# Optimization experiments

Measured on AMD Instinct MI355X. Metric: run time of the kernel, lower is better.

## Reference

```python
import jax, jax.numpy as jnp
import numpy as np

V, NB, NJ, NP, NK = 6890, 10, 24, 207, 19
PARENTS = np.array([-1, 0, 0, 0, 1, 2, 3, 4, 5, 6, 7, 8, 9, 9, 9, 12, 13, 14, 16, 17, 18, 19, 20, 21])


def setup_inputs():
    key = jax.random.key(0)
    ks = jax.random.split(key, 9)
    B = 1024
    beta = jax.random.normal(ks[0], (B, NB), jnp.float32)
    theta = jax.random.normal(ks[1], (B, NJ * 3), jnp.float32) * 0.3  # axis-angle per joint
    trans = jax.random.normal(ks[2], (B, 3), jnp.float32)
    v_template = jax.random.normal(ks[3], (V, 3), jnp.float32)
    shapedirs = jax.random.normal(ks[4], (NB, V * 3), jnp.float32) * 0.03
    Jr = jax.random.uniform(ks[5], (V, NJ), jnp.float32)
    J_regressor = Jr / jnp.sum(Jr, axis=0, keepdims=True)
    posedirs = jax.random.normal(ks[6], (NP, V * 3), jnp.float32) * 0.01
    jr = jax.random.uniform(ks[7], (V, NK), jnp.float32)
    joint_regressor = jr / jnp.sum(jr, axis=0, keepdims=True)
    w = jax.random.uniform(ks[8], (V, NJ), jnp.float32)
    weights = w / jnp.sum(w, axis=1, keepdims=True)  # LBS weights, rows sum to 1
    return dict(beta=beta, theta=theta, trans=trans, v_template=v_template,
                shapedirs=shapedirs, J_regressor=J_regressor, posedirs=posedirs,
                joint_regressor=joint_regressor, weights=weights)


def batch_rodrigues(theta):
    # theta: (N,3) axis-angle -> (N,3,3) rotation matrices via quaternions (HMR-style)
    angle = jnp.linalg.norm(theta + 1e-8, axis=1, keepdims=True)
    half = angle * 0.5
    v = (theta / angle) * jnp.sin(half)
    quat = jnp.concatenate([jnp.cos(half), v], axis=1)
    quat = quat / jnp.linalg.norm(quat, axis=1, keepdims=True)
    w, x, y, z = quat[:, 0], quat[:, 1], quat[:, 2], quat[:, 3]
    rot = jnp.stack([
        1 - 2 * (y * y + z * z), 2 * (x * y - w * z), 2 * (x * z + w * y),
        2 * (x * y + w * z), 1 - 2 * (x * x + z * z), 2 * (y * z - w * x),
        2 * (x * z - w * y), 2 * (y * z + w * x), 1 - 2 * (x * x + y * y)], axis=1)
    return rot.reshape(-1, 3, 3)


def batch_global_rigid_transformation(Rs, J):
    # Rs: (B,24,3,3), J: (B,24,3); rotate_base=True
    B = Rs.shape[0]
    rot_x = jnp.array([[1., 0., 0.], [0., -1., 0.], [0., 0., -1.]], jnp.float32)
    root_R = Rs[:, 0] @ rot_x

    def make_A(R, t):  # (B,3,3),(B,3) -> (B,4,4)
        top = jnp.concatenate([R, t[:, :, None]], axis=2)
        bot = jnp.broadcast_to(jnp.array([0., 0., 0., 1.], jnp.float32), (B, 1, 4))
        return jnp.concatenate([top, bot], axis=1)

    results = [make_A(root_R, J[:, 0])]
    for i in range(1, NJ):  # fixed 24-joint kinematic chain
        t = J[:, i] - J[:, PARENTS[i]]
        results.append(results[PARENTS[i]] @ make_A(Rs[:, i], t))
    res = jnp.stack(results, axis=1)  # (B,24,4,4)
    new_J = res[:, :, :3, 3]
    j_w0 = jnp.concatenate([J, jnp.zeros_like(J[:, :, :1])], axis=2)  # (B,24,4), homo w=0
    init_bone = jnp.einsum('bjrc,bjc->bjr', res, j_w0)
    A = res.at[:, :, :, 3].add(-init_bone)  # subtract only last column (matches F.pad trick)
    return new_J, A


def reference(beta, theta, trans, v_template, shapedirs, J_regressor, posedirs, joint_regressor, weights):
    B = beta.shape[0]
    v_shaped = (beta @ shapedirs).reshape(B, V, 3) + v_template
    J = jnp.einsum('bvc,vj->bjc', v_shaped, J_regressor)  # (B,24,3)
    Rs = batch_rodrigues(theta.reshape(-1, 3)).reshape(B, NJ, 3, 3)
    pose_feature = (Rs[:, 1:] - jnp.eye(3, dtype=Rs.dtype)).reshape(B, NP)
    v_posed = (pose_feature @ posedirs).reshape(B, V, 3) + v_shaped
    _, A = batch_global_rigid_transformation(Rs, J)
    T = jnp.einsum('vj,bjrc->bvrc', weights, A)  # (B,V,4,4) per-vertex skinning transforms
    homo = jnp.concatenate([v_posed, jnp.ones((B, V, 1), v_posed.dtype)], axis=2)
    verts = jnp.einsum('bvrc,bvc->bvr', T, homo)[:, :, :3] + trans[:, None, :]
    joints = jnp.einsum('bvc,vk->bkc', verts, joint_regressor)  # (B,19,3)
    return joints
```

## Files before the change

### kernel.cpp

```cpp
#include <hip/hip_runtime.h>
#include <hip/hip_bf16.h>

constexpr int Vn   = 6890;
constexpr int VC3  = 20670;
constexpr int NKB  = 216;
constexpr int QT   = 224;
constexpr int NMG  = 14;
constexpr int NCOL = 480;
constexpr int WR   = 1440;
constexpr int MC   = 1368;
constexpr int KSEG = 8;
constexpr int RB   = 158;

using bf16x8  = __attribute__((ext_vector_type(8))) short;
using floatx4 = __attribute__((ext_vector_type(4))) float;

__device__ __forceinline__ unsigned short f2bf(float f) {
    unsigned int u = __float_as_uint(f);
    unsigned int r = (u + 0x7FFFu + ((u >> 16) & 1u)) >> 16;
    return (unsigned short)r;
}

__global__ __launch_bounds__(256) void k0_build(
    const float* __restrict__ vt, const float* __restrict__ sdirs,
    const float* __restrict__ pdirs, const float* __restrict__ Jreg,
    const float* __restrict__ jreg, const float* __restrict__ wts,
    unsigned short* __restrict__ Af, unsigned short* __restrict__ Bf,
    float* __restrict__ Jacc)
{
    int bx = blockIdx.x, t = threadIdx.x;
    if (bx < 756) {
        int g = bx * 256 + t;
        int q = g / 864, u = g % 864;
        int v0 = u * 8, base = 3 * v0;
        float buf[24];
        if (q == 0) {
            #pragma unroll
            for (int i = 0; i < 24; ++i) buf[i] = (v0 + i / 3 < Vn) ? 1.f : 0.f;
        } else {
            const float* src = nullptr;
            if (q == 1) src = vt;
            else if (q >= 2 && q < 12)   src = sdirs + (size_t)(q - 2) * VC3;
            else if (q >= 12 && q < 219) src = pdirs + (size_t)(q - 12) * VC3;
            if (src && base + 23 < VC3) {
                #pragma unroll
                for (int i = 0; i < 12; ++i) {
                    float2 f = *(const float2*)(src + base + 2 * i);
                    buf[2 * i] = f.x; buf[2 * i + 1] = f.y;
                }
            } else {
                #pragma unroll
                for (int i = 0; i < 24; ++i)
                    buf[i] = (src && base + i < VC3) ? src[base + i] : 0.f;
            }
        }
        int kb = u >> 2, quad = u & 3, mg = q >> 4;
        size_t foff = (size_t)((q & 15) + quad * 16) * 8;
        #pragma unroll
        for (int c = 0; c < 3; ++c) {
            bf16x8 o;
            #pragma unroll
            for (int j = 0; j < 8; ++j) o[j] = (short)f2bf(buf[3 * j + c]);
            *(bf16x8*)(Af + ((size_t)(c * NMG + mg) * NKB + kb) * 512 + foff) = o;
        }
        return;
    }
    bx -= 756;
    if (bx < 108) {
        int v0 = bx * 64;
        __shared__ float js[64 * 19], wsh[64 * 24], Jsh[64 * 24];
        for (int i = t; i < 64 * 19; i += 256)
            js[i] = (v0 * 19 + i < Vn * 19) ? jreg[v0 * 19 + i] : 0.f;
        for (int i = t; i < 64 * 24; i += 256) {
            wsh[i] = (v0 * 24 + i < Vn * 24) ? wts[v0 * 24 + i] : 0.f;
            Jsh[i] = (v0 * 24 + i < Vn * 24) ? Jreg[v0 * 24 + i] : 0.f;
        }
        __syncthreads();
        for (int s = t; s < 4096; s += 256) {
            int col = s >> 3, vg = s & 7;
            int kb = (v0 >> 5) + (vg >> 2);
            bf16x8 o;
            #pragma unroll
            for (int j = 0; j < 8; ++j) {
                int vl = vg * 8 + j;
                float val = 0.f;
                if (col < 456)      val = js[vl * 19 + col / 24] * wsh[vl * 24 + col % 24];
                else if (col < 480) val = Jsh[vl * 24 + (col - 456)];
                o[j] = (short)f2bf(val);
            }
            *(bf16x8*)(Bf + ((size_t)(col >> 4) * NKB + kb) * 512
                          + (size_t)((col & 15) + (vg & 3) * 16) * 8) = o;
        }
        return;
    }
    for (int i = t; i < 792; i += 256) Jacc[i] = 0.f;
}

__device__ __forceinline__ void k1_load(bf16x8 (&a)[2], bf16x8 (&b)[4],
    const unsigned short* __restrict__ ap, const unsigned short* __restrict__ bp, int i)
{
    a[0] = *(const bf16x8*)(ap + (size_t)(0 * NKB + i) * 512);
    a[1] = *(const bf16x8*)(ap + (size_t)(1 * NKB + i) * 512);
    b[0] = *(const bf16x8*)(bp + (size_t)(0 * NKB + i) * 512);
    b[1] = *(const bf16x8*)(bp + (size_t)(1 * NKB + i) * 512);
    b[2] = *(const bf16x8*)(bp + (size_t)(2 * NKB + i) * 512);
    b[3] = *(const bf16x8*)(bp + (size_t)(3 * NKB + i) * 512);
}

__global__ __launch_bounds__(64) void k1_mfma(
    const unsigned short* __restrict__ Af, const unsigned short* __restrict__ Bf,
    float* __restrict__ P, float* __restrict__ Jacc)
{
    int l = threadIdx.x;
    int wid = blockIdx.x;
    int kseg = wid / 168; int r = wid % 168;
    int c = r / 56; r %= 56;
    int mt = r >> 3, nt = r & 7;
    int kb0 = kseg * 27;

    const unsigned short* ap = Af + ((size_t)(c * NMG + mt * 2) * NKB + kb0) * 512 + l * 8;
    const unsigned short* bp = Bf + ((size_t)(nt * 4) * NKB + kb0) * 512 + l * 8;

    floatx4 acc[2][4];
    #pragma unroll
    for (int mi = 0; mi < 2; ++mi)
        #pragma unroll
        for (int ni = 0; ni < 4; ++ni) acc[mi][ni] = floatx4{0.f, 0.f, 0.f, 0.f};

    bf16x8 a[4][2], b[4][4];
    k1_load(a[0], b[0], ap, bp, 0);
    k1_load(a[1], b[1], ap, bp, 1);
    k1_load(a[2], b[2], ap, bp, 2);
    #pragma unroll
    for (int i = 0; i < 27; ++i) {
        int pf = (i + 3 < 27) ? i + 3 : 26;
        k1_load(a[(i + 3) & 3], b[(i + 3) & 3], ap, bp, pf);
        bf16x8 (&ac)[2] = a[i & 3];
        bf16x8 (&bc)[4] = b[i & 3];
        #pragma unroll
        for (int mi = 0; mi < 2; ++mi)
            #pragma unroll
            for (int ni = 0; ni < 4; ++ni)
                acc[mi][ni] = __builtin_amdgcn_mfma_f32_16x16x32_bf16(ac[mi], bc[ni], acc[mi][ni], 0, 0, 0);
    }
    float* Ps = P + (size_t)kseg * WR * QT;
    int lr = l & 15, rq = (l >> 4) * 4;
    #pragma unroll
    for (int mi = 0; mi < 2; ++mi)
        #pragma unroll
        for (int ni = 0; ni < 4; ++ni) {
            int col = nt * 64 + ni * 16 + lr;
            if (col < NCOL) {
                int q0 = mt * 32 + mi * 16 + rq;
                *(floatx4*)(Ps + (size_t)(col * 3 + c) * QT + q0) = acc[mi][ni];
            }
        }
    if (mt == 0 && nt == 7 && rq < 12) {
        #pragma unroll
        for (int ni = 0; ni < 2; ++ni) {
            int col = 448 + ni * 16 + lr;
            if (col >= 456 && col < 480) {
                #pragma unroll
                for (int rr = 0; rr < 4; ++rr) {
                    int q = rq + rr;
                    if (q >= 1 && q < 12)
                        atomicAdd(&Jacc[(size_t)((col - 456) * 3 + c) * 11 + (q - 1)],
                                  acc[0][ni][rr]);
                }
            }
        }
    }
}

__global__ __launch_bounds__(256) void k12_reduce_prep(
    const float* __restrict__ P, const float* __restrict__ Jacc,
    const float* __restrict__ beta, const float* __restrict__ theta,
    unsigned short* __restrict__ Wb3, float* __restrict__ w1g,
    unsigned short* __restrict__ xbf, float* __restrict__ RAg, float* __restrict__ tAg)
{
    int t = threadIdx.x;
    if (blockIdx.x < RB) {
        int g = blockIdx.x * 256 + t;
        if (g >= WR * 28) return;
        int colc = g / 28, q0 = (g % 28) * 8;
        float v[8] = {0, 0, 0, 0, 0, 0, 0, 0};
        #pragma unroll
        for (int s = 0; s < KSEG; ++s) {
            const float4* p = (const float4*)(P + ((size_t)s * WR + colc) * QT + q0);
            float4 x0 = p[0], x1 = p[1];
            v[0] += x0.x; v[1] += x0.y; v[2] += x0.z; v[3] += x0.w;
            v[4] += x1.x; v[5] += x1.y; v[6] += x1.z; v[7] += x1.w;
        }
        if (colc < 1408) {
            bf16x8 o;
            #pragma unroll
            for (int j = 0; j < 8; ++j)
                o[j] = (short)((colc < MC) ? f2bf(v[j]) : 0);
            *(bf16x8*)(Wb3 + ((size_t)(colc >> 4) * 7 + (q0 >> 5)) * 512
                           + (size_t)((colc & 15) + ((q0 >> 3) & 3) * 16) * 8) = o;
        }
        if (q0 == 0 && colc % 3 == 0 && colc < MC) w1g[colc / 3] = v[0];
        return;
    }
    int b = blockIdx.x - RB;
    __shared__ float Rs[24][9];
    __shared__ float Jl[24][3];
    __shared__ float resR[24][9];
    __shared__ float rest[24][3];
    __shared__ float bet[10];

    if (t < 10) bet[t] = beta[b * 10 + t];
    if (t < 24) {
        float t0 = theta[b * 72 + t * 3 + 0];
        float t1 = theta[b * 72 + t * 3 + 1];
        float t2 = theta[b * 72 + t * 3 + 2];
        float e0 = t0 + 1e-8f, e1 = t1 + 1e-8f, e2 = t2 + 1e-8f;
        float angle = sqrtf(e0 * e0 + e1 * e1 + e2 * e2);
        float half = 0.5f * angle;
        float sh = sinf(half), ch = cosf(half);
        float s = sh / angle;
        float qx = t0 * s, qy = t1 * s, qz = t2 * s;
        float qn = sqrtf(ch * ch + qx * qx + qy * qy + qz * qz);
        float w = ch / qn, x = qx / qn, y = qy / qn, z = qz / qn;
        Rs[t][0] = 1.f - 2.f * (y * y + z * z);
        Rs[t][1] = 2.f * (x * y - w * z);
        Rs[t][2] = 2.f * (x * z + w * y);
        Rs[t][3] = 2.f * (x * y + w * z);
        Rs[t][4] = 1.f - 2.f * (x * x + z * z);
        Rs[t][5] = 2.f * (y * z - w * x);
        Rs[t][6] = 2.f * (x * z - w * y);
        Rs[t][7] = 2.f * (y * z + w * x);
        Rs[t][8] = 1.f - 2.f * (x * x + y * y);
    }
    __syncthreads();
    if (t < 72) {
        const float* basep = Jacc + (size_t)t * 11;
        float acc = basep[0];
        #pragma unroll
        for (int n = 0; n < 10; ++n) acc += bet[n] * basep[1 + n];
        Jl[t / 3][t % 3] = acc;
    }
    for (int q = t; q < QT; q += 256) {
        float xv = 0.f;
        if (q == 1) xv = 1.f;
        else if (q >= 2 && q < 12) xv = bet[q - 2];
        else if (q >= 12 && q < 219) {
            int p = q - 12;
            int jj = 1 + p / 9, e = p % 9;
            float rr = Rs[jj][e];
            if (e == 0 || e == 4 || e == 8) rr -= 1.f;
            xv = rr;
        }
        xbf[((size_t)(b >> 4) * 7 + (q >> 5)) * 512
            + (size_t)((b & 15) + ((q >> 3) & 3) * 16) * 8 + (q & 7)] = f2bf(xv);
    }
    __syncthreads();
    if (t == 0) {
        const int par[24] = {-1,0,0,0,1,2,3,4,5,6,7,8,9,9,9,12,13,14,16,17,18,19,20,21};
        #pragma unroll
        for (int rr = 0; rr < 3; ++rr) {
            resR[0][rr * 3 + 0] =  Rs[0][rr * 3 + 0];
            resR[0][rr * 3 + 1] = -Rs[0][rr * 3 + 1];
            resR[0][rr * 3 + 2] = -Rs[0][rr * 3 + 2];
            rest[0][rr] = Jl[0][rr];
        }
        for (int i = 1; i < 24; ++i) {
            int p = par[i];
            float t0 = Jl[i][0] - Jl[p][0];
            float t1 = Jl[i][1] - Jl[p][1];
            float t2 = Jl[i][2] - Jl[p][2];
            #pragma unroll
            for (int rr = 0; rr < 3; ++rr) {
                float a0 = resR[p][rr * 3 + 0], a1 = resR[p][rr * 3 + 1], a2 = resR[p][rr * 3 + 2];
                resR[i][rr * 3 + 0] = a0 * Rs[i][0] + a1 * Rs[i][3] + a2 * Rs[i][6];
                resR[i][rr * 3 + 1] = a0 * Rs[i][1] + a1 * Rs[i][4] + a2 * Rs[i][7];
                resR[i][rr * 3 + 2] = a0 * Rs[i][2] + a1 * Rs[i][5] + a2 * Rs[i][8];
                rest[i][rr] = a0 * t0 + a1 * t1 + a2 * t2 + rest[p][rr];
            }
        }
    }
    __syncthreads();
    if (t < 216) RAg[(size_t)b * 216 + t] = resR[t / 9][t % 9];
    if (t < 72) {
        int j = t / 3, c = t % 3;
        tAg[(size_t)b * 72 + t] = rest[j][c]
            - (resR[j][c * 3 + 0] * Jl[j][0] + resR[j][c * 3 + 1] * Jl[j][1]
             + resR[j][c * 3 + 2] * Jl[j][2]);
    }
}

__global__ __launch_bounds__(256) void k3_mfma(
    const unsigned short* __restrict__ Wb3, const unsigned short* __restrict__ xbf,
    float* __restrict__ Mg)
{
    int w = threadIdx.x >> 6, l = threadIdx.x & 63;
    int wm = w & 1, wn = w >> 1;
    int ct = blockIdx.x % 22, bt = blockIdx.x / 22;
    int mg0 = ct * 4 + wm * 2;
    int bg0 = bt * 8 + wn * 4;
    const unsigned short* ap = Wb3 + (size_t)mg0 * 7 * 512 + l * 8;
    const unsigned short* bp = xbf + (size_t)bg0 * 7 * 512 + l * 8;

    floatx4 acc[2][4];
    #pragma unroll
    for (int mi = 0; mi < 2; ++mi)
        #pragma unroll
        for (int ni = 0; ni < 4; ++ni) acc[mi][ni] = floatx4{0.f, 0.f, 0.f, 0.f};

    #pragma unroll
    for (int kk = 0; kk < 7; ++kk) {
        bf16x8 a0 = *(const bf16x8*)(ap + (size_t)(0 * 7 + kk) * 512);
        bf16x8 a1 = *(const bf16x8*)(ap + (size_t)(1 * 7 + kk) * 512);
        bf16x8 b0 = *(const bf16x8*)(bp + (size_t)(0 * 7 + kk) * 512);
        bf16x8 b1 = *(const bf16x8*)(bp + (size_t)(1 * 7 + kk) * 512);
        bf16x8 b2 = *(const bf16x8*)(bp + (size_t)(2 * 7 + kk) * 512);
        bf16x8 b3 = *(const bf16x8*)(bp + (size_t)(3 * 7 + kk) * 512);
        acc[0][0] = __builtin_amdgcn_mfma_f32_16x16x32_bf16(a0, b0, acc[0][0], 0, 0, 0);
        acc[0][1] = __builtin_amdgcn_mfma_f32_16x16x32_bf16(a0, b1, acc[0][1], 0, 0, 0);
        acc[0][2] = __builtin_amdgcn_mfma_f32_16x16x32_bf16(a0, b2, acc[0][2], 0, 0, 0);
        acc[0][3] = __builtin_amdgcn_mfma_f32_16x16x32_bf16(a0, b3, acc[0][3], 0, 0, 0);
        acc[1][0] = __builtin_amdgcn_mfma_f32_16x16x32_bf16(a1, b0, acc[1][0], 0, 0, 0);
        acc[1][1] = __builtin_amdgcn_mfma_f32_16x16x32_bf16(a1, b1, acc[1][1], 0, 0, 0);
        acc[1][2] = __builtin_amdgcn_mfma_f32_16x16x32_bf16(a1, b2, acc[1][2], 0, 0, 0);
        acc[1][3] = __builtin_amdgcn_mfma_f32_16x16x32_bf16(a1, b3, acc[1][3], 0, 0, 0);
    }
    int lr = l & 15, rq = (l >> 4) * 4;
    #pragma unroll
    for (int mi = 0; mi < 2; ++mi)
        #pragma unroll
        for (int ni = 0; ni < 4; ++ni) {
            int b  = bt * 128 + wn * 64 + ni * 16 + lr;
            int cc = (mg0 + mi) * 16 + rq;
            if (cc < MC)
                *(floatx4*)(Mg + (size_t)b * MC + cc) = acc[mi][ni];
        }
}

__global__ __launch_bounds__(256) void k4_combine(
    const float* __restrict__ Mg, const float* __restrict__ RAg,
    const float* __restrict__ tAg, const float* __restrict__ w1g,
    const float* __restrict__ trans, float* __restrict__ out)
{
    __shared__ float w1s[456];
    __shared__ float Ms[4 * MC];
    __shared__ float RAs[4 * 216];
    __shared__ float tAs[4 * 72];
    int tid = threadIdx.x;
    int b0 = blockIdx.x * 4;
    for (int i = tid; i < 456; i += 256) w1s[i] = w1g[i];
    for (int i = tid; i < 4 * MC; i += 256) Ms[i] = Mg[(size_t)b0 * MC + i];
    for (int i = tid; i < 4 * 216; i += 256) RAs[i] = RAg[(size_t)b0 * 216 + i];
    for (int i = tid; i < 4 * 72; i += 256) tAs[i] = tAg[(size_t)b0 * 72 + i];
    __syncthreads();
    if (tid < 228) {
        int lb = tid / 57, kc = tid % 57;
        int k = kc / 3, c = kc % 3;
        int b = b0 + lb;
        float acc = trans[b * 3 + c];
        const float* Mrow = Ms + lb * MC;
        const float* RAr  = RAs + lb * 216;
        const float* tAr  = tAs + lb * 72;
        #pragma unroll
        for (int j = 0; j < 24; ++j) {
            int kj = k * 24 + j;
            float m0 = Mrow[kj * 3 + 0], m1 = Mrow[kj * 3 + 1], m2 = Mrow[kj * 3 + 2];
            acc += RAr[j * 9 + c * 3 + 0] * m0
                 + RAr[j * 9 + c * 3 + 1] * m1
                 + RAr[j * 9 + c * 3 + 2] * m2
                 + tAr[j * 3 + c] * w1s[kj];
        }
        out[b * 57 + kc] = acc;
    }
}

extern "C" void kernel_launch(void* const* d_in, const int* in_sizes, int n_in,
                              void* d_out, int out_size, void* d_ws, size_t ws_size,
                              hipStream_t stream)
{
    const float* beta  = (const float*)d_in[0];
    const float* theta = (const float*)d_in[1];
    const float* trans = (const float*)d_in[2];
    const float* vt    = (const float*)d_in[3];
    const float* sdirs = (const float*)d_in[4];
    const float* Jreg  = (const float*)d_in[5];
    const float* pdirs = (const float*)d_in[6];
    const float* jreg  = (const float*)d_in[7];
    const float* wts   = (const float*)d_in[8];
    float* out = (float*)d_out;
    int B = in_sizes[0] / 10;

    unsigned short* Af  = (unsigned short*)d_ws;
    unsigned short* Bf  = Af + (size_t)3 * NMG * NKB * 512;
    unsigned short* Wb3 = Bf + (size_t)32 * NKB * 512;
    unsigned short* xbf = Wb3 + (size_t)88 * 7 * 512;
    float* P    = (float*)(xbf + (size_t)64 * 7 * 512);
    float* Jacc = P + (size_t)KSEG * WR * QT;
    float* w1g  = Jacc + 792;
    float* RAg  = w1g + 456;
    float* tAg  = RAg + (size_t)B * 216;
    float* Mg   = tAg + (size_t)B * 72;

    k0_build<<<dim3(756 + 108 + 1), 256, 0, stream>>>(
        vt, sdirs, pdirs, Jreg, jreg, wts, Af, Bf, Jacc);
    k1_mfma<<<dim3(168 * KSEG), 64, 0, stream>>>(Af, Bf, P, Jacc);
    k12_reduce_prep<<<dim3(RB + B), 256, 0, stream>>>(
        P, Jacc, beta, theta, Wb3, w1g, xbf, RAg, tAg);
    k3_mfma<<<dim3((B / 128) * 22), 256, 0, stream>>>(Wb3, xbf, Mg);
    k4_combine<<<dim3(B / 4), 256, 0, stream>>>(Mg, RAg, tAg, w1g, trans, out);
}
```

Measured before the change: 147.9 us.

## Merge coordinate axis into M tile and rebalance K split in k1 GEMM

k1_mfma now folds the three coordinate groups into a single padded M dimension of 704 rows, so each wave computes a 64x64 output tile instead of 32x64. This raises operand reuse per loaded fragment. The K split goes from 8 segments of 27 blocks to 18 segments of 12, and the deeper 3-stage register prefetch is replaced by a double buffer. k0_build gains blocks that zero the padded A rows. The trade-off is a larger partial-sum buffer P that k12 must write and then reduce, plus higher register pressure from 64 accumulators per lane.

```diff
diff --git a/kernel.cpp b/kernel.cpp
--- a/kernel.cpp
+++ b/kernel.cpp
@@ -6,10 +6,12 @@
 constexpr int NKB  = 216;
 constexpr int QT   = 224;
 constexpr int NMG  = 14;
+constexpr int AMG  = 44;
 constexpr int NCOL = 480;
 constexpr int WR   = 1440;
 constexpr int MC   = 1368;
-constexpr int KSEG = 8;
+constexpr int KSEG = 18;
+constexpr int KCH  = 12;
 constexpr int RB   = 158;
 
 using bf16x8  = __attribute__((ext_vector_type(8))) short;
@@ -93,18 +95,13 @@
         }
         return;
     }
+    bx -= 108;
+    if (bx < 108) {
+        bf16x8 z = {0, 0, 0, 0, 0, 0, 0, 0};
+        *(bf16x8*)(Af + (size_t)42 * NKB * 512 + ((size_t)bx * 256 + t) * 8) = z;
+        return;
+    }
     for (int i = t; i < 792; i += 256) Jacc[i] = 0.f;
-}
-
-__device__ __forceinline__ void k1_load(bf16x8 (&a)[2], bf16x8 (&b)[4],
-    const unsigned short* __restrict__ ap, const unsigned short* __restrict__ bp, int i)
-{
-    a[0] = *(const bf16x8*)(ap + (size_t)(0 * NKB + i) * 512);
-    a[1] = *(const bf16x8*)(ap + (size_t)(1 * NKB + i) * 512);
-    b[0] = *(const bf16x8*)(bp + (size_t)(0 * NKB + i) * 512);
-    b[1] = *(const bf16x8*)(bp + (size_t)(1 * NKB + i) * 512);
-    b[2] = *(const bf16x8*)(bp + (size_t)(2 * NKB + i) * 512);
-    b[3] = *(const bf16x8*)(bp + (size_t)(3 * NKB + i) * 512);
 }
 
 __global__ __launch_bounds__(64) void k1_mfma(
@@ -113,59 +110,83 @@
 {
     int l = threadIdx.x;
     int wid = blockIdx.x;
-    int kseg = wid / 168; int r = wid % 168;
-    int c = r / 56; r %= 56;
+    int kseg = wid / 88; int r = wid % 88;
     int mt = r >> 3, nt = r & 7;
-    int kb0 = kseg * 27;
-
-    const unsigned short* ap = Af + ((size_t)(c * NMG + mt * 2) * NKB + kb0) * 512 + l * 8;
+    int kb0 = kseg * KCH;
+
+    const unsigned short* ap = Af + ((size_t)(mt * 4) * NKB + kb0) * 512 + l * 8;
     const unsigned short* bp = Bf + ((size_t)(nt * 4) * NKB + kb0) * 512 + l * 8;
 
-    floatx4 acc[2][4];
-    #pragma unroll
-    for (int mi = 0; mi < 2; ++mi)
+    floatx4 acc[4][4];
+    #pragma unroll
+    for (int mi = 0; mi < 4; ++mi)
         #pragma unroll
         for (int ni = 0; ni < 4; ++ni) acc[mi][ni] = floatx4{0.f, 0.f, 0.f, 0.f};
 
-    bf16x8 a[4][2], b[4][4];
-    k1_load(a[0], b[0], ap, bp, 0);
-    k1_load(a[1], b[1], ap, bp, 1);
-    k1_load(a[2], b[2], ap, bp, 2);
-    #pragma unroll
-    for (int i = 0; i < 27; ++i) {
-        int pf = (i + 3 < 27) ? i + 3 : 26;
-        k1_load(a[(i + 3) & 3], b[(i + 3) & 3], ap, bp, pf);
-        bf16x8 (&ac)[2] = a[i & 3];
-        bf16x8 (&bc)[4] = b[i & 3];
-        #pragma unroll
-        for (int mi = 0; mi < 2; ++mi)
+    bf16x8 a[2][4], b[2][4];
+    #pragma unroll
+    for (int mi = 0; mi < 4; ++mi)
+        a[0][mi] = *(const bf16x8*)(ap + (size_t)mi * NKB * 512);
+    #pragma unroll
+    for (int ni = 0; ni < 4; ++ni)
+        b[0][ni] = *(const bf16x8*)(bp + (size_t)ni * NKB * 512);
+
+    #pragma unroll
+    for (int i = 0; i < KCH; ++i) {
+        int s = i & 1;
+        if (i + 1 < KCH) {
+            #pragma unroll
+            for (int mi = 0; mi < 4; ++mi)
+                a[s ^ 1][mi] = *(const bf16x8*)(ap + ((size_t)mi * NKB + i + 1) * 512);
             #pragma unroll
             for (int ni = 0; ni < 4; ++ni)
-                acc[mi][ni] = __builtin_amdgcn_mfma_f32_16x16x32_bf16(ac[mi], bc[ni], acc[mi][ni], 0, 0, 0);
-    }
+                b[s ^ 1][ni] = *(const bf16x8*)(bp + ((size_t)ni * NKB + i + 1) * 512);
+        }
+        #pragma unroll
+        for (int mi = 0; mi < 4; ++mi)
+            #pragma unroll
+            for (int ni = 0; ni < 4; ++ni)
+                acc[mi][ni] = __builtin_amdgcn_mfma_f32_16x16x32_bf16(
+                    a[s][mi], b[s][ni], acc[mi][ni], 0, 0, 0);
+    }
+
     float* Ps = P + (size_t)kseg * WR * QT;
     int lr = l & 15, rq = (l >> 4) * 4;
     #pragma unroll
-    for (int mi = 0; mi < 2; ++mi)
-        #pragma unroll
-        for (int ni = 0; ni < 4; ++ni) {
-            int col = nt * 64 + ni * 16 + lr;
-            if (col < NCOL) {
-                int q0 = mt * 32 + mi * 16 + rq;
-                *(floatx4*)(Ps + (size_t)(col * 3 + c) * QT + q0) = acc[mi][ni];
+    for (int mi = 0; mi < 4; ++mi) {
+        int row = mt * 64 + mi * 16 + rq;
+        if (row < 672) {
+            int c = row / 224;
+            int q0 = row - c * 224;
+            #pragma unroll
+            for (int ni = 0; ni < 4; ++ni) {
+                int col = nt * 64 + ni * 16 + lr;
+                if (col < NCOL)
+                    *(floatx4*)(Ps + (size_t)(col * 3 + c) * QT + q0) = acc[mi][ni];
             }
         }
-    if (mt == 0 && nt == 7 && rq < 12) {
-        #pragma unroll
-        for (int ni = 0; ni < 2; ++ni) {
-            int col = 448 + ni * 16 + lr;
-            if (col >= 456 && col < 480) {
-                #pragma unroll
-                for (int rr = 0; rr < 4; ++rr) {
-                    int q = rq + rr;
-                    if (q >= 1 && q < 12)
-                        atomicAdd(&Jacc[(size_t)((col - 456) * 3 + c) * 11 + (q - 1)],
-                                  acc[0][ni][rr]);
+    }
+    if (nt == 7 && (mt == 0 || mt == 3 || mt == 7)) {
+        #pragma unroll
+        for (int mi = 0; mi < 4; ++mi) {
+            int row = mt * 64 + mi * 16 + rq;
+            if (row < 672) {
+                int c = row / 224;
+                int q0 = row - c * 224;
+                if (q0 < 12) {
+                    #pragma unroll
+                    for (int ni = 0; ni < 4; ++ni) {
+                        int col = nt * 64 + ni * 16 + lr;
+                        if (col >= 456 && col < 480) {
+                            #pragma unroll
+                            for (int rr = 0; rr < 4; ++rr) {
+                                int q = q0 + rr;
+                                if (q >= 1 && q < 12)
+                                    atomicAdd(&Jacc[(size_t)((col - 456) * 3 + c) * 11 + (q - 1)],
+                                              acc[mi][ni][rr]);
+                            }
+                        }
+                    }
                 }
             }
         }
@@ -390,7 +411,7 @@
     int B = in_sizes[0] / 10;
 
     unsigned short* Af  = (unsigned short*)d_ws;
-    unsigned short* Bf  = Af + (size_t)3 * NMG * NKB * 512;
+    unsigned short* Bf  = Af + (size_t)AMG * NKB * 512;
     unsigned short* Wb3 = Bf + (size_t)32 * NKB * 512;
     unsigned short* xbf = Wb3 + (size_t)88 * 7 * 512;
     float* P    = (float*)(xbf + (size_t)64 * 7 * 512);
@@ -400,9 +421,9 @@
     float* tAg  = RAg + (size_t)B * 216;
     float* Mg   = tAg + (size_t)B * 72;
 
-    k0_build<<<dim3(756 + 108 + 1), 256, 0, stream>>>(
+    k0_build<<<dim3(756 + 108 + 109), 256, 0, stream>>>(
         vt, sdirs, pdirs, Jreg, jreg, wts, Af, Bf, Jacc);
-    k1_mfma<<<dim3(168 * KSEG), 64, 0, stream>>>(Af, Bf, P, Jacc);
+    k1_mfma<<<dim3(88 * KSEG), 64, 0, stream>>>(Af, Bf, P, Jacc);
     k12_reduce_prep<<<dim3(RB + B), 256, 0, stream>>>(
         P, Jacc, beta, theta, Wb3, w1g, xbf, RAg, tAg);
     k3_mfma<<<dim3((B / 128) * 22), 256, 0, stream>>>(Wb3, xbf, Mg);
```

Measured after the change: 155.1 us. +4.9%, slower.

## Fuse four post-build kernels into one persistent kernel with grid barriers

Applied to the files above, without the earlier changes.

Replaces the k1, k12, k3 and k4 launches with a single persistent kernel of 336 blocks that runs each stage in turn, separated by atomic-counter grid barriers. The barrier counter is reset in the build kernel. The aim is to remove launch gaps and tail effects between the small stages. In exchange, the work per stage is remapped: per-batch prep now uses one wave per batch element, and the spin barriers rely on all 336 blocks being co-resident, which is a deadlock risk if occupancy does not allow it.

```diff
diff --git a/kernel.cpp b/kernel.cpp
--- a/kernel.cpp
+++ b/kernel.cpp
@@ -10,7 +10,7 @@
 constexpr int WR   = 1440;
 constexpr int MC   = 1368;
 constexpr int KSEG = 8;
-constexpr int RB   = 158;
+constexpr int NBLK = 336;
 
 using bf16x8  = __attribute__((ext_vector_type(8))) short;
 using floatx4 = __attribute__((ext_vector_type(4))) float;
@@ -26,7 +26,7 @@
     const float* __restrict__ pdirs, const float* __restrict__ Jreg,
     const float* __restrict__ jreg, const float* __restrict__ wts,
     unsigned short* __restrict__ Af, unsigned short* __restrict__ Bf,
-    float* __restrict__ Jacc)
+    float* __restrict__ Jacc, unsigned* __restrict__ bar)
 {
     int bx = blockIdx.x, t = threadIdx.x;
     if (bx < 756) {
@@ -94,6 +94,17 @@
         return;
     }
     for (int i = t; i < 792; i += 256) Jacc[i] = 0.f;
+    if (t == 0) bar[0] = 0u;
+}
+
+__device__ __forceinline__ void gbar(unsigned* bar, unsigned target) {
+    __syncthreads();
+    if (threadIdx.x == 0) {
+        __hip_atomic_fetch_add(&bar[0], 1u, __ATOMIC_ACQ_REL, __HIP_MEMORY_SCOPE_AGENT);
+        while (__hip_atomic_load(&bar[0], __ATOMIC_ACQUIRE, __HIP_MEMORY_SCOPE_AGENT) < target)
+            __builtin_amdgcn_s_sleep(2);
+    }
+    __syncthreads();
 }
 
 __device__ __forceinline__ void k1_load(bf16x8 (&a)[2], bf16x8 (&b)[4],
@@ -107,12 +118,10 @@
     b[3] = *(const bf16x8*)(bp + (size_t)(3 * NKB + i) * 512);
 }
 
-__global__ __launch_bounds__(64) void k1_mfma(
+__device__ void k1_wave(int wid, int l,
     const unsigned short* __restrict__ Af, const unsigned short* __restrict__ Bf,
     float* __restrict__ P, float* __restrict__ Jacc)
 {
-    int l = threadIdx.x;
-    int wid = blockIdx.x;
     int kseg = wid / 168; int r = wid % 168;
     int c = r / 56; r %= 56;
     int mt = r >> 3, nt = r & 7;
@@ -172,204 +181,218 @@
     }
 }
 
-__global__ __launch_bounds__(256) void k12_reduce_prep(
-    const float* __restrict__ P, const float* __restrict__ Jacc,
+__global__ __launch_bounds__(256, 2) void mega(
+    const unsigned short* __restrict__ Af, const unsigned short* __restrict__ Bf,
+    float* __restrict__ P, float* __restrict__ Jacc,
     const float* __restrict__ beta, const float* __restrict__ theta,
     unsigned short* __restrict__ Wb3, float* __restrict__ w1g,
-    unsigned short* __restrict__ xbf, float* __restrict__ RAg, float* __restrict__ tAg)
+    unsigned short* __restrict__ xbf, float* __restrict__ RAg, float* __restrict__ tAg,
+    float* __restrict__ Mg, const float* __restrict__ trans, float* __restrict__ out,
+    unsigned* __restrict__ bar)
 {
+    __shared__ __align__(16) float smem[7080];
     int t = threadIdx.x;
-    if (blockIdx.x < RB) {
+
+    {
+        int wid = blockIdx.x * 4 + (t >> 6);
+        k1_wave(wid, t & 63, Af, Bf, P, Jacc);
+    }
+    gbar(bar, NBLK);
+
+    {
         int g = blockIdx.x * 256 + t;
-        if (g >= WR * 28) return;
-        int colc = g / 28, q0 = (g % 28) * 8;
-        float v[8] = {0, 0, 0, 0, 0, 0, 0, 0};
-        #pragma unroll
-        for (int s = 0; s < KSEG; ++s) {
-            const float4* p = (const float4*)(P + ((size_t)s * WR + colc) * QT + q0);
-            float4 x0 = p[0], x1 = p[1];
-            v[0] += x0.x; v[1] += x0.y; v[2] += x0.z; v[3] += x0.w;
-            v[4] += x1.x; v[5] += x1.y; v[6] += x1.z; v[7] += x1.w;
-        }
-        if (colc < 1408) {
-            bf16x8 o;
-            #pragma unroll
-            for (int j = 0; j < 8; ++j)
-                o[j] = (short)((colc < MC) ? f2bf(v[j]) : 0);
-            *(bf16x8*)(Wb3 + ((size_t)(colc >> 4) * 7 + (q0 >> 5)) * 512
-                           + (size_t)((colc & 15) + ((q0 >> 3) & 3) * 16) * 8) = o;
-        }
-        if (q0 == 0 && colc % 3 == 0 && colc < MC) w1g[colc / 3] = v[0];
-        return;
-    }
-    int b = blockIdx.x - RB;
-    __shared__ float Rs[24][9];
-    __shared__ float Jl[24][3];
-    __shared__ float resR[24][9];
-    __shared__ float rest[24][3];
-    __shared__ float bet[10];
-
-    if (t < 10) bet[t] = beta[b * 10 + t];
-    if (t < 24) {
-        float t0 = theta[b * 72 + t * 3 + 0];
-        float t1 = theta[b * 72 + t * 3 + 1];
-        float t2 = theta[b * 72 + t * 3 + 2];
-        float e0 = t0 + 1e-8f, e1 = t1 + 1e-8f, e2 = t2 + 1e-8f;
-        float angle = sqrtf(e0 * e0 + e1 * e1 + e2 * e2);
-        float half = 0.5f * angle;
-        float sh = sinf(half), ch = cosf(half);
-        float s = sh / angle;
-        float qx = t0 * s, qy = t1 * s, qz = t2 * s;
-        float qn = sqrtf(ch * ch + qx * qx + qy * qy + qz * qz);
-        float w = ch / qn, x = qx / qn, y = qy / qn, z = qz / qn;
-        Rs[t][0] = 1.f - 2.f * (y * y + z * z);
-        Rs[t][1] = 2.f * (x * y - w * z);
-        Rs[t][2] = 2.f * (x * z + w * y);
-        Rs[t][3] = 2.f * (x * y + w * z);
-        Rs[t][4] = 1.f - 2.f * (x * x + z * z);
-        Rs[t][5] = 2.f * (y * z - w * x);
-        Rs[t][6] = 2.f * (x * z - w * y);
-        Rs[t][7] = 2.f * (y * z + w * x);
-        Rs[t][8] = 1.f - 2.f * (x * x + y * y);
-    }
-    __syncthreads();
-    if (t < 72) {
-        const float* basep = Jacc + (size_t)t * 11;
-        float acc = basep[0];
-        #pragma unroll
-        for (int n = 0; n < 10; ++n) acc += bet[n] * basep[1 + n];
-        Jl[t / 3][t % 3] = acc;
-    }
-    for (int q = t; q < QT; q += 256) {
-        float xv = 0.f;
-        if (q == 1) xv = 1.f;
-        else if (q >= 2 && q < 12) xv = bet[q - 2];
-        else if (q >= 12 && q < 219) {
-            int p = q - 12;
-            int jj = 1 + p / 9, e = p % 9;
-            float rr = Rs[jj][e];
-            if (e == 0 || e == 4 || e == 8) rr -= 1.f;
-            xv = rr;
-        }
-        xbf[((size_t)(b >> 4) * 7 + (q >> 5)) * 512
-            + (size_t)((b & 15) + ((q >> 3) & 3) * 16) * 8 + (q & 7)] = f2bf(xv);
-    }
-    __syncthreads();
-    if (t == 0) {
-        const int par[24] = {-1,0,0,0,1,2,3,4,5,6,7,8,9,9,9,12,13,14,16,17,18,19,20,21};
-        #pragma unroll
-        for (int rr = 0; rr < 3; ++rr) {
-            resR[0][rr * 3 + 0] =  Rs[0][rr * 3 + 0];
-            resR[0][rr * 3 + 1] = -Rs[0][rr * 3 + 1];
-            resR[0][rr * 3 + 2] = -Rs[0][rr * 3 + 2];
-            rest[0][rr] = Jl[0][rr];
-        }
-        for (int i = 1; i < 24; ++i) {
-            int p = par[i];
-            float t0 = Jl[i][0] - Jl[p][0];
-            float t1 = Jl[i][1] - Jl[p][1];
-            float t2 = Jl[i][2] - Jl[p][2];
+        if (g < WR * 28) {
+            int colc = g / 28, q0 = (g % 28) * 8;
+            float v[8] = {0, 0, 0, 0, 0, 0, 0, 0};
+            #pragma unroll
+            for (int s = 0; s < KSEG; ++s) {
+                const float4* p = (const float4*)(P + ((size_t)s * WR + colc) * QT + q0);
+                float4 x0 = p[0], x1 = p[1];
+                v[0] += x0.x; v[1] += x0.y; v[2] += x0.z; v[3] += x0.w;
+                v[4] += x1.x; v[5] += x1.y; v[6] += x1.z; v[7] += x1.w;
+            }
+            if (colc < 1408) {
+                bf16x8 o;
+                #pragma unroll
+                for (int j = 0; j < 8; ++j)
+                    o[j] = (short)((colc < MC) ? f2bf(v[j]) : 0);
+                *(bf16x8*)(Wb3 + ((size_t)(colc >> 4) * 7 + (q0 >> 5)) * 512
+                               + (size_t)((colc & 15) + ((q0 >> 3) & 3) * 16) * 8) = o;
+            }
+            if (q0 == 0 && colc % 3 == 0 && colc < MC) w1g[colc / 3] = v[0];
+        }
+    }
+    if (blockIdx.x < 256) {
+        int widx = t >> 6, l = t & 63;
+        int b = blockIdx.x * 4 + widx;
+        float* Rs   = smem + widx * 640;
+        float* Jl   = Rs + 216;
+        float* resR = Jl + 72;
+        float* rest = resR + 216;
+        float* bet  = rest + 72;
+
+        if (l < 10) bet[l] = beta[b * 10 + l];
+        if (l < 24) {
+            float t0 = theta[b * 72 + l * 3 + 0];
+            float t1 = theta[b * 72 + l * 3 + 1];
+            float t2 = theta[b * 72 + l * 3 + 2];
+            float e0 = t0 + 1e-8f, e1 = t1 + 1e-8f, e2 = t2 + 1e-8f;
+            float angle = sqrtf(e0 * e0 + e1 * e1 + e2 * e2);
+            float half = 0.5f * angle;
+            float sh = sinf(half), ch = cosf(half);
+            float s = sh / angle;
+            float qx = t0 * s, qy = t1 * s, qz = t2 * s;
+            float qn = sqrtf(ch * ch + qx * qx + qy * qy + qz * qz);
+            float w = ch / qn, x = qx / qn, y = qy / qn, z = qz / qn;
+            Rs[l * 9 + 0] = 1.f - 2.f * (y * y + z * z);
+            Rs[l * 9 + 1] = 2.f * (x * y - w * z);
+            Rs[l * 9 + 2] = 2.f * (x * z + w * y);
+            Rs[l * 9 + 3] = 2.f * (x * y + w * z);
+            Rs[l * 9 + 4] = 1.f - 2.f * (x * x + z * z);
+            Rs[l * 9 + 5] = 2.f * (y * z - w * x);
+            Rs[l * 9 + 6] = 2.f * (x * z - w * y);
+            Rs[l * 9 + 7] = 2.f * (y * z + w * x);
+            Rs[l * 9 + 8] = 1.f - 2.f * (x * x + y * y);
+        }
+        __syncthreads();
+        if (l < 64) {
+            for (int idx = l; idx < 72; idx += 64) {
+                const float* basep = Jacc + (size_t)idx * 11;
+                float acc = basep[0];
+                #pragma unroll
+                for (int n = 0; n < 10; ++n) acc += bet[n] * basep[1 + n];
+                Jl[idx] = acc;
+            }
+        }
+        for (int q = l; q < QT; q += 64) {
+            float xv = 0.f;
+            if (q == 1) xv = 1.f;
+            else if (q >= 2 && q < 12) xv = bet[q - 2];
+            else if (q >= 12 && q < 219) {
+                int p = q - 12;
+                int jj = 1 + p / 9, e = p % 9;
+                float rr = Rs[jj * 9 + e];
+                if (e == 0 || e == 4 || e == 8) rr -= 1.f;
+                xv = rr;
+            }
+            xbf[((size_t)(b >> 4) * 7 + (q >> 5)) * 512
+                + (size_t)((b & 15) + ((q >> 3) & 3) * 16) * 8 + (q & 7)] = f2bf(xv);
+        }
+        __syncthreads();
+        if (l == 0) {
+            const int par[24] = {-1,0,0,0,1,2,3,4,5,6,7,8,9,9,9,12,13,14,16,17,18,19,20,21};
             #pragma unroll
             for (int rr = 0; rr < 3; ++rr) {
-                float a0 = resR[p][rr * 3 + 0], a1 = resR[p][rr * 3 + 1], a2 = resR[p][rr * 3 + 2];
-                resR[i][rr * 3 + 0] = a0 * Rs[i][0] + a1 * Rs[i][3] + a2 * Rs[i][6];
-                resR[i][rr * 3 + 1] = a0 * Rs[i][1] + a1 * Rs[i][4] + a2 * Rs[i][7];
-                resR[i][rr * 3 + 2] = a0 * Rs[i][2] + a1 * Rs[i][5] + a2 * Rs[i][8];
-                rest[i][rr] = a0 * t0 + a1 * t1 + a2 * t2 + rest[p][rr];
-            }
-        }
-    }
-    __syncthreads();
-    if (t < 216) RAg[(size_t)b * 216 + t] = resR[t / 9][t % 9];
-    if (t < 72) {
-        int j = t / 3, c = t % 3;
-        tAg[(size_t)b * 72 + t] = rest[j][c]
-            - (resR[j][c * 3 + 0] * Jl[j][0] + resR[j][c * 3 + 1] * Jl[j][1]
-             + resR[j][c * 3 + 2] * Jl[j][2]);
-    }
-}
-
-__global__ __launch_bounds__(256) void k3_mfma(
-    const unsigned short* __restrict__ Wb3, const unsigned short* __restrict__ xbf,
-    float* __restrict__ Mg)
-{
-    int w = threadIdx.x >> 6, l = threadIdx.x & 63;
-    int wm = w & 1, wn = w >> 1;
-    int ct = blockIdx.x % 22, bt = blockIdx.x / 22;
-    int mg0 = ct * 4 + wm * 2;
-    int bg0 = bt * 8 + wn * 4;
-    const unsigned short* ap = Wb3 + (size_t)mg0 * 7 * 512 + l * 8;
-    const unsigned short* bp = xbf + (size_t)bg0 * 7 * 512 + l * 8;
-
-    floatx4 acc[2][4];
-    #pragma unroll
-    for (int mi = 0; mi < 2; ++mi)
-        #pragma unroll
-        for (int ni = 0; ni < 4; ++ni) acc[mi][ni] = floatx4{0.f, 0.f, 0.f, 0.f};
-
-    #pragma unroll
-    for (int kk = 0; kk < 7; ++kk) {
-        bf16x8 a0 = *(const bf16x8*)(ap + (size_t)(0 * 7 + kk) * 512);
-        bf16x8 a1 = *(const bf16x8*)(ap + (size_t)(1 * 7 + kk) * 512);
-        bf16x8 b0 = *(const bf16x8*)(bp + (size_t)(0 * 7 + kk) * 512);
-        bf16x8 b1 = *(const bf16x8*)(bp + (size_t)(1 * 7 + kk) * 512);
-        bf16x8 b2 = *(const bf16x8*)(bp + (size_t)(2 * 7 + kk) * 512);
-        bf16x8 b3 = *(const bf16x8*)(bp + (size_t)(3 * 7 + kk) * 512);
-        acc[0][0] = __builtin_amdgcn_mfma_f32_16x16x32_bf16(a0, b0, acc[0][0], 0, 0, 0);
-        acc[0][1] = __builtin_amdgcn_mfma_f32_16x16x32_bf16(a0, b1, acc[0][1], 0, 0, 0);
-        acc[0][2] = __builtin_amdgcn_mfma_f32_16x16x32_bf16(a0, b2, acc[0][2], 0, 0, 0);
-        acc[0][3] = __builtin_amdgcn_mfma_f32_16x16x32_bf16(a0, b3, acc[0][3], 0, 0, 0);
-        acc[1][0] = __builtin_amdgcn_mfma_f32_16x16x32_bf16(a1, b0, acc[1][0], 0, 0, 0);
-        acc[1][1] = __builtin_amdgcn_mfma_f32_16x16x32_bf16(a1, b1, acc[1][1], 0, 0, 0);
-        acc[1][2] = __builtin_amdgcn_mfma_f32_16x16x32_bf16(a1, b2, acc[1][2], 0, 0, 0);
-        acc[1][3] = __builtin_amdgcn_mfma_f32_16x16x32_bf16(a1, b3, acc[1][3], 0, 0, 0);
-    }
-    int lr = l & 15, rq = (l >> 4) * 4;
-    #pragma unroll
-    for (int mi = 0; mi < 2; ++mi)
-        #pragma unroll
-        for (int ni = 0; ni < 4; ++ni) {
-            int b  = bt * 128 + wn * 64 + ni * 16 + lr;
-            int cc = (mg0 + mi) * 16 + rq;
-            if (cc < MC)
-                *(floatx4*)(Mg + (size_t)b * MC + cc) = acc[mi][ni];
-        }
-}
-
-__global__ __launch_bounds__(256) void k4_combine(
-    const float* __restrict__ Mg, const float* __restrict__ RAg,
-    const float* __restrict__ tAg, const float* __restrict__ w1g,
-    const float* __restrict__ trans, float* __restrict__ out)
-{
-    __shared__ float w1s[456];
-    __shared__ float Ms[4 * MC];
-    __shared__ float RAs[4 * 216];
-    __shared__ float tAs[4 * 72];
-    int tid = threadIdx.x;
-    int b0 = blockIdx.x * 4;
-    for (int i = tid; i < 456; i += 256) w1s[i] = w1g[i];
-    for (int i = tid; i < 4 * MC; i += 256) Ms[i] = Mg[(size_t)b0 * MC + i];
-    for (int i = tid; i < 4 * 216; i += 256) RAs[i] = RAg[(size_t)b0 * 216 + i];
-    for (int i = tid; i < 4 * 72; i += 256) tAs[i] = tAg[(size_t)b0 * 72 + i];
-    __syncthreads();
-    if (tid < 228) {
-        int lb = tid / 57, kc = tid % 57;
-        int k = kc / 3, c = kc % 3;
-        int b = b0 + lb;
-        float acc = trans[b * 3 + c];
-        const float* Mrow = Ms + lb * MC;
-        const float* RAr  = RAs + lb * 216;
-        const float* tAr  = tAs + lb * 72;
-        #pragma unroll
-        for (int j = 0; j < 24; ++j) {
-            int kj = k * 24 + j;
-            float m0 = Mrow[kj * 3 + 0], m1 = Mrow[kj * 3 + 1], m2 = Mrow[kj * 3 + 2];
-            acc += RAr[j * 9 + c * 3 + 0] * m0
-                 + RAr[j * 9 + c * 3 + 1] * m1
-                 + RAr[j * 9 + c * 3 + 2] * m2
-                 + tAr[j * 3 + c] * w1s[kj];
-        }
-        out[b * 57 + kc] = acc;
+                resR[0 * 9 + rr * 3 + 0] =  Rs[rr * 3 + 0];
+                resR[0 * 9 + rr * 3 + 1] = -Rs[rr * 3 + 1];
+                resR[0 * 9 + rr * 3 + 2] = -Rs[rr * 3 + 2];
+                rest[rr] = Jl[rr];
+            }
+            for (int i = 1; i < 24; ++i) {
+                int p = par[i];
+                float t0 = Jl[i * 3 + 0] - Jl[p * 3 + 0];
+                float t1 = Jl[i * 3 + 1] - Jl[p * 3 + 1];
+                float t2 = Jl[i * 3 + 2] - Jl[p * 3 + 2];
+                #pragma unroll
+                for (int rr = 0; rr < 3; ++rr) {
+                    float a0 = resR[p * 9 + rr * 3 + 0], a1 = resR[p * 9 + rr * 3 + 1], a2 = resR[p * 9 + rr * 3 + 2];
+                    resR[i * 9 + rr * 3 + 0] = a0 * Rs[i * 9 + 0] + a1 * Rs[i * 9 + 3] + a2 * Rs[i * 9 + 6];
+                    resR[i * 9 + rr * 3 + 1] = a0 * Rs[i * 9 + 1] + a1 * Rs[i * 9 + 4] + a2 * Rs[i * 9 + 7];
+                    resR[i * 9 + rr * 3 + 2] = a0 * Rs[i * 9 + 2] + a1 * Rs[i * 9 + 5] + a2 * Rs[i * 9 + 8];
+                    rest[i * 3 + rr] = a0 * t0 + a1 * t1 + a2 * t2 + rest[p * 3 + rr];
+                }
+            }
+        }
+        __syncthreads();
+        for (int idx = l; idx < 216; idx += 64)
+            RAg[(size_t)b * 216 + idx] = resR[idx];
+        if (l < 72) {
+            int j = l / 3, c = l % 3;
+            tAg[(size_t)b * 72 + l] = rest[j * 3 + c]
+                - (resR[j * 9 + c * 3 + 0] * Jl[j * 3 + 0] + resR[j * 9 + c * 3 + 1] * Jl[j * 3 + 1]
+                 + resR[j * 9 + c * 3 + 2] * Jl[j * 3 + 2]);
+        }
+    }
+    gbar(bar, 2 * NBLK);
+
+    {
+        int wt = blockIdx.x * 4 + (t >> 6);
+        if (wt < 704) {
+            int blk = wt >> 2, w = wt & 3, l = t & 63;
+            int wm = w & 1, wn = w >> 1;
+            int ct = blk % 22, bt = blk / 22;
+            int mg0 = ct * 4 + wm * 2;
+            int bg0 = bt * 8 + wn * 4;
+            const unsigned short* ap = Wb3 + (size_t)mg0 * 7 * 512 + l * 8;
+            const unsigned short* bp = xbf + (size_t)bg0 * 7 * 512 + l * 8;
+
+            floatx4 acc[2][4];
+            #pragma unroll
+            for (int mi = 0; mi < 2; ++mi)
+                #pragma unroll
+                for (int ni = 0; ni < 4; ++ni) acc[mi][ni] = floatx4{0.f, 0.f, 0.f, 0.f};
+
+            #pragma unroll
+            for (int kk = 0; kk < 7; ++kk) {
+                bf16x8 a0 = *(const bf16x8*)(ap + (size_t)(0 * 7 + kk) * 512);
+                bf16x8 a1 = *(const bf16x8*)(ap + (size_t)(1 * 7 + kk) * 512);
+                bf16x8 b0 = *(const bf16x8*)(bp + (size_t)(0 * 7 + kk) * 512);
+                bf16x8 b1 = *(const bf16x8*)(bp + (size_t)(1 * 7 + kk) * 512);
+                bf16x8 b2 = *(const bf16x8*)(bp + (size_t)(2 * 7 + kk) * 512);
+                bf16x8 b3 = *(const bf16x8*)(bp + (size_t)(3 * 7 + kk) * 512);
+                acc[0][0] = __builtin_amdgcn_mfma_f32_16x16x32_bf16(a0, b0, acc[0][0], 0, 0, 0);
+                acc[0][1] = __builtin_amdgcn_mfma_f32_16x16x32_bf16(a0, b1, acc[0][1], 0, 0, 0);
+                acc[0][2] = __builtin_amdgcn_mfma_f32_16x16x32_bf16(a0, b2, acc[0][2], 0, 0, 0);
+                acc[0][3] = __builtin_amdgcn_mfma_f32_16x16x32_bf16(a0, b3, acc[0][3], 0, 0, 0);
+                acc[1][0] = __builtin_amdgcn_mfma_f32_16x16x32_bf16(a1, b0, acc[1][0], 0, 0, 0);
+                acc[1][1] = __builtin_amdgcn_mfma_f32_16x16x32_bf16(a1, b1, acc[1][1], 0, 0, 0);
+                acc[1][2] = __builtin_amdgcn_mfma_f32_16x16x32_bf16(a1, b2, acc[1][2], 0, 0, 0);
+                acc[1][3] = __builtin_amdgcn_mfma_f32_16x16x32_bf16(a1, b3, acc[1][3], 0, 0, 0);
+            }
+            int lr = l & 15, rq = (l >> 4) * 4;
+            #pragma unroll
+            for (int mi = 0; mi < 2; ++mi)
+                #pragma unroll
+                for (int ni = 0; ni < 4; ++ni) {
+                    int b  = bt * 128 + wn * 64 + ni * 16 + lr;
+                    int cc = (mg0 + mi) * 16 + rq;
+                    if (cc < MC)
+                        *(floatx4*)(Mg + (size_t)b * MC + cc) = acc[mi][ni];
+                }
+        }
+    }
+    gbar(bar, 3 * NBLK);
+
+    if (blockIdx.x < 256) {
+        float* w1s = smem;
+        float* Ms  = smem + 456;
+        float* RAs = smem + 5928;
+        float* tAs = smem + 6792;
+        int b0 = blockIdx.x * 4;
+        for (int i = t; i < 456; i += 256) w1s[i] = w1g[i];
+        for (int i = t; i < 4 * MC; i += 256) Ms[i] = Mg[(size_t)b0 * MC + i];
+        for (int i = t; i < 4 * 216; i += 256) RAs[i] = RAg[(size_t)b0 * 216 + i];
+        for (int i = t; i < 4 * 72; i += 256) tAs[i] = tAg[(size_t)b0 * 72 + i];
+        __syncthreads();
+        if (t < 228) {
+            int lb = t / 57, kc = t % 57;
+            int k = kc / 3, c = kc % 3;
+            int b = b0 + lb;
+            float acc = trans[b * 3 + c];
+            const float* Mrow = Ms + lb * MC;
+            const float* RAr  = RAs + lb * 216;
+            const float* tAr  = tAs + lb * 72;
+            #pragma unroll
+            for (int j = 0; j < 24; ++j) {
+                int kj = k * 24 + j;
+                float m0 = Mrow[kj * 3 + 0], m1 = Mrow[kj * 3 + 1], m2 = Mrow[kj * 3 + 2];
+                acc += RAr[j * 9 + c * 3 + 0] * m0
+                     + RAr[j * 9 + c * 3 + 1] * m1
+                     + RAr[j * 9 + c * 3 + 2] * m2
+                     + tAr[j * 3 + c] * w1s[kj];
+            }
+            out[b * 57 + kc] = acc;
+        }
     }
 }
 
@@ -390,7 +413,7 @@
     int B = in_sizes[0] / 10;
 
     unsigned short* Af  = (unsigned short*)d_ws;
-    unsigned short* Bf  = Af + (size_t)3 * NMG * NKB * 512;
+    unsigned short* Bf  = Af + (size_t)42 * NKB * 512;
     unsigned short* Wb3 = Bf + (size_t)32 * NKB * 512;
     unsigned short* xbf = Wb3 + (size_t)88 * 7 * 512;
     float* P    = (float*)(xbf + (size_t)64 * 7 * 512);
@@ -399,12 +422,10 @@
     float* RAg  = w1g + 456;
     float* tAg  = RAg + (size_t)B * 216;
     float* Mg   = tAg + (size_t)B * 72;
+    unsigned* bar = (unsigned*)(Mg + (size_t)B * MC);
 
     k0_build<<<dim3(756 + 108 + 1), 256, 0, stream>>>(
-        vt, sdirs, pdirs, Jreg, jreg, wts, Af, Bf, Jacc);
-    k1_mfma<<<dim3(168 * KSEG), 64, 0, stream>>>(Af, Bf, P, Jacc);
-    k12_reduce_prep<<<dim3(RB + B), 256, 0, stream>>>(
-        P, Jacc, beta, theta, Wb3, w1g, xbf, RAg, tAg);
-    k3_mfma<<<dim3((B / 128) * 22), 256, 0, stream>>>(Wb3, xbf, Mg);
-    k4_combine<<<dim3(B / 4), 256, 0, stream>>>(Mg, RAg, tAg, w1g, trans, out);
-}
+        vt, sdirs, pdirs, Jreg, jreg, wts, Af, Bf, Jacc, bar);
+    mega<<<dim3(NBLK), 256, 0, stream>>>(
+        Af, Bf, P, Jacc, beta, theta, Wb3, w1g, xbf, RAg, tAg, Mg, trans, out, bar);
+}
```

Result: slower. 265.3 us (+79.3%).
